# Optimization experiments

Hardware: AMD Instinct MI355X
Metric: run time of the kernel (lower is better)

## Reference

```python
import jax, jax.numpy as jnp
import numpy as np
import math

B, S, L, H, NH, FF, V = 32, 512, 12, 768, 12, 3072, 30522
DH = H // NH


def setup_inputs() -> dict:
    key = jax.random.key(0)
    ks = jax.random.split(key, 16)
    w = lambda k, shape: (jax.random.normal(k, shape, jnp.float32) * 0.02)
    return {
        "input_ids": jax.random.randint(ks[0], (B, S), 0, V, dtype=jnp.int32),
        "attention_mask": jax.random.uniform(ks[1], (B, S), jnp.float32),
        "word_emb": w(ks[2], (V, H)),
        "pos_emb": w(ks[3], (S, H)),
        "type_emb": w(ks[4], (H,)),
        "ln_emb_s": jnp.ones((H,), jnp.float32),
        "ln_emb_b": jnp.zeros((H,), jnp.float32),
        "Wq": w(ks[5], (L, H, H)), "bq": jnp.zeros((L, H), jnp.float32),
        "Wk": w(ks[6], (L, H, H)), "bk": jnp.zeros((L, H), jnp.float32),
        "Wv": w(ks[7], (L, H, H)), "bv": jnp.zeros((L, H), jnp.float32),
        "Wo": w(ks[8], (L, H, H)), "bo": jnp.zeros((L, H), jnp.float32),
        "ln1_s": jnp.ones((L, H), jnp.float32), "ln1_b": jnp.zeros((L, H), jnp.float32),
        "Wi": w(ks[9], (L, H, FF)), "bi": jnp.zeros((L, FF), jnp.float32),
        "Wf": w(ks[10], (L, FF, H)), "bf": jnp.zeros((L, H), jnp.float32),
        "ln2_s": jnp.ones((L, H), jnp.float32), "ln2_b": jnp.zeros((L, H), jnp.float32),
    }


def _ln(x, s, b):
    # BERT LayerNorm, eps=1e-12
    m = jnp.mean(x, -1, keepdims=True)
    v = jnp.mean((x - m) ** 2, -1, keepdims=True)
    return (x - m) * jax.lax.rsqrt(v + 1e-12) * s + b


def reference(input_ids, attention_mask, word_emb, pos_emb, type_emb,
              ln_emb_s, ln_emb_b, Wq, bq, Wk, bk, Wv, bv, Wo, bo,
              ln1_s, ln1_b, Wi, bi, Wf, bf, ln2_s, ln2_b):
    b, s = input_ids.shape
    scale = 1.0 / math.sqrt(DH)
    # Embeddings: word + position + (single) token-type, then LayerNorm
    h = word_emb[input_ids] + pos_emb[None, :s] + type_emb
    h = _ln(h, ln_emb_s, ln_emb_b)
    key_mask = attention_mask[:, None, None, :]  # [B,1,1,S], float

    def layer(h, p):
        wq, bq_, wk, bk_, wv, bv_, wo, bo_, l1s, l1b, wi, bi_, wf, bf_, l2s, l2b = p
        q = (jnp.einsum('bsd,de->bse', h, wq) + bq_).reshape(b, s, NH, DH)
        k = (jnp.einsum('bsd,de->bse', h, wk) + bk_).reshape(b, s, NH, DH)
        v = (jnp.einsum('bsd,de->bse', h, wv) + bv_).reshape(b, s, NH, DH)
        scores = jnp.einsum('bqhd,bkhd->bhqk', q, k) * scale
        probs = jax.nn.softmax(scores, axis=-1)
        # post-softmax masking + renormalization (the non-standard part)
        probs = probs * key_mask
        probs = probs / jnp.clip(jnp.sum(probs, -1, keepdims=True), 1e-9, None)
        ctx = jnp.einsum('bhqk,bkhd->bqhd', probs, v).reshape(b, s, H)
        attn_out = _ln(jnp.einsum('bsd,de->bse', ctx, wo) + bo_ + h, l1s, l1b)
        inter = jax.nn.gelu(jnp.einsum('bsd,df->bsf', attn_out, wi) + bi_, approximate=False)
        out = _ln(jnp.einsum('bsf,fd->bsd', inter, wf) + bf_ + attn_out, l2s, l2b)
        return out, None

    h, _ = jax.lax.scan(layer, h, (Wq, bq, Wk, bk, Wv, bv, Wo, bo,
                                   ln1_s, ln1_b, Wi, bi, Wf, bf, ln2_s, ln2_b))
    # masked mean pooling + L2 normalize (normalize=True)
    m = attention_mask[..., None]
    sent = jnp.sum(h * m, axis=1) / jnp.clip(jnp.sum(m, axis=1), 1e-6, None)
    sent = sent / jnp.clip(jnp.linalg.norm(sent, axis=-1, keepdims=True), 1e-12, None)
    return sent
```

## Files before the change

kernel.cpp:

```cpp
#include <hip/hip_runtime.h>
#include <hip/hip_bf16.h>
#include <math.h>

typedef __bf16 bf16;
typedef __bf16 bf16x8 __attribute__((ext_vector_type(8)));
typedef float  f32x4  __attribute__((ext_vector_type(4)));

#define B_  32
#define S_  512
#define H_  768
#define NH_ 12
#define DH_ 64
#define FF_ 3072
#define L_  12
#define M_  (B_*S_)
#define QKV_ 2304

#define KST 68
#define VST 516
#define PST 68

__device__ __forceinline__ void gload16(const bf16* g, bf16* l) {
  __builtin_amdgcn_global_load_lds(
      (const __attribute__((address_space(1))) void*)g,
      (__attribute__((address_space(3))) void*)l, 16, 0, 0);
}

__device__ __forceinline__ float fast_gelu(float x) {
  float z = x * 0.70710678118f;
  float s = fabsf(z);
  float t = __builtin_amdgcn_rcpf(1.0f + 0.3275911f * s);
  float p = t*(0.254829592f + t*(-0.284496736f + t*(1.421413741f +
            t*(-1.453152027f + t*1.061405429f))));
  float e = p * __expf(-s*s);
  float erfv = copysignf(1.0f - e, z);
  return 0.5f * x * (1.0f + erfv);
}

__global__ __launch_bounds__(512, 4) void gemm128(
    const bf16* __restrict__ A, const bf16* __restrict__ Bt,
    const float* __restrict__ bias, void* __restrict__ outp,
    int N, int K, int tiles_n, int epi)
{
  __shared__ bf16 As[128*64];
  __shared__ bf16 Bs[128*64];
  const int tid  = threadIdx.x;
  const int lane = tid & 63, wid = tid >> 6;
  const int wr = wid >> 2, wc = wid & 3;
  const int lrow = lane & 15, kgrp = lane >> 4;

  const int nwg = gridDim.x, orig = blockIdx.x;
  const int qc = nwg >> 3, rc = nwg & 7;
  const int xcd = orig & 7, lin = orig >> 3;
  const int wg = (xcd < rc ? xcd*(qc+1) : rc*(qc+1) + (xcd-rc)*qc) + lin;
  const int tm = wg / tiles_n, tn = wg % tiles_n;
  const size_t m0 = (size_t)tm * 128, n0 = (size_t)tn * 128;
  const int KT = K >> 6;

  const bf16* Ab = A  + m0 * K;
  const bf16* Bb = Bt + n0 * K;

  auto stage = [&](const bf16* gbase, bf16* ldsbase, int kt) {
#pragma unroll
    for (int j = 0; j < 2; ++j) {
      int lin2  = j*512 + tid;
      int prow  = lin2 >> 3;
      int pslot = lin2 & 7;
      int lslot = pslot ^ (prow & 7);
      const bf16* src = gbase + (size_t)prow * K + (size_t)kt*64 + lslot*8;
      bf16* dst = ldsbase + (size_t)(j*512 + (wid<<6))*8;
      gload16(src, dst);
    }
  };

  f32x4 acc[4][2] = {};

  for (int t = 0; t < KT; ++t) {
    __syncthreads();
    stage(Ab, As, t);
    stage(Bb, Bs, t);
    __syncthreads();
#pragma unroll
    for (int kk = 0; kk < 2; ++kk) {
      bf16x8 a[4], b[2];
#pragma unroll
      for (int m = 0; m < 4; ++m) {
        int row  = wr*64 + m*16 + lrow;
        int slot = (kk*4 + kgrp) ^ (lrow & 7);
        a[m] = *(const bf16x8*)&As[row*64 + slot*8];
      }
#pragma unroll
      for (int n = 0; n < 2; ++n) {
        int row  = wc*32 + n*16 + lrow;
        int slot = (kk*4 + kgrp) ^ (lrow & 7);
        b[n] = *(const bf16x8*)&Bs[row*64 + slot*8];
      }
#pragma unroll
      for (int m = 0; m < 4; ++m)
#pragma unroll
        for (int n = 0; n < 2; ++n)
          acc[m][n] = __builtin_amdgcn_mfma_f32_16x16x32_bf16(a[m], b[n], acc[m][n], 0, 0, 0);
    }
  }

#pragma unroll
  for (int m = 0; m < 4; ++m)
#pragma unroll
    for (int n = 0; n < 2; ++n) {
      int col = (int)n0 + wc*32 + n*16 + lrow;
      float bv = bias[col];
#pragma unroll
      for (int r = 0; r < 4; ++r) {
        int row = (int)m0 + wr*64 + m*16 + kgrp*4 + r;
        float x = acc[m][n][r] + bv;
        size_t idx = (size_t)row * N + col;
        if (epi == 1)      ((float*)outp)[idx] = x;
        else if (epi == 0) ((bf16*)outp)[idx]  = (bf16)x;
        else               ((bf16*)outp)[idx]  = (bf16)fast_gelu(x);
      }
    }
}

__global__ __launch_bounds__(256) void weight_prep(
    const float* __restrict__ Wq, const float* __restrict__ Wk,
    const float* __restrict__ Wv, const float* __restrict__ Wo,
    const float* __restrict__ Wi, const float* __restrict__ Wf,
    const float* __restrict__ bq, const float* __restrict__ bk,
    const float* __restrict__ bv,
    bf16* __restrict__ wqkv, bf16* __restrict__ wot,
    bf16* __restrict__ wit,  bf16* __restrict__ wft,
    float* __restrict__ qkbias)
{
  int bid = blockIdx.x;
  if (bid >= 1728) {
    int i = (bid - 1728)*256 + threadIdx.x;
    if (i < QKV_)
      qkbias[i] = (i < 768) ? bq[i] : (i < 1536 ? bk[i-768] : bv[i-1536]);
    return;
  }
  const float* W; bf16* Wt; int K, N, t;
  if (bid < 576) {
    K = 768; N = 768;
    if      (bid < 144) { W = Wq; Wt = wqkv;             t = bid; }
    else if (bid < 288) { W = Wk; Wt = wqkv + 768*768;   t = bid - 144; }
    else if (bid < 432) { W = Wv; Wt = wqkv + 2*768*768; t = bid - 288; }
    else                { W = Wo; Wt = wot;              t = bid - 432; }
  } else if (bid < 1152) { W = Wi; Wt = wit; K = 768;  N = 3072; t = bid - 576; }
  else                   { W = Wf; Wt = wft; K = 3072; N = 768;  t = bid - 1152; }
  const int kt = K >> 6;
  const int k0 = (t % kt)*64, n0 = (t / kt)*64;

  __shared__ bf16 T[64][65];
  int tx = threadIdx.x & 63, ty = threadIdx.x >> 6;
#pragma unroll
  for (int j = 0; j < 16; ++j) {
    int kk = j*4 + ty;
    T[kk][tx] = (bf16)W[(size_t)(k0+kk)*N + n0 + tx];
  }
  __syncthreads();
#pragma unroll
  for (int j = 0; j < 16; ++j) {
    int nn = j*4 + ty;
    Wt[(size_t)(n0+nn)*K + k0 + tx] = T[tx][nn];
  }
}

__device__ __forceinline__ void block_sum2(float& a, float& b, float* red) {
  int lane = threadIdx.x & 63, wid = threadIdx.x >> 6;
  for (int o = 32; o > 0; o >>= 1) { a += __shfl_xor(a, o); b += __shfl_xor(b, o); }
  if (lane == 0) { red[wid*2] = a; red[wid*2+1] = b; }
  __syncthreads();
  a = red[0] + red[2] + red[4] + red[6];
  b = red[1] + red[3] + red[5] + red[7];
  __syncthreads();
}

__global__ __launch_bounds__(256) void embed_ln(
    const int* __restrict__ ids, const float* __restrict__ we,
    const float* __restrict__ pe, const float* __restrict__ te,
    const float* __restrict__ gs, const float* __restrict__ gb,
    float* __restrict__ h32, bf16* __restrict__ hb)
{
  __shared__ float red[8];
  int row = blockIdx.x;
  int s = row & (S_-1);
  int id = ids[row];
  int t = threadIdx.x;
  float x[3], sum = 0.f, sq = 0.f;
#pragma unroll
  for (int j = 0; j < 3; ++j) {
    int c = t + j*256;
    float v = we[(size_t)id*H_ + c] + pe[(size_t)s*H_ + c] + te[c];
    x[j] = v; sum += v; sq += v*v;
  }
  block_sum2(sum, sq, red);
  float mean = sum * (1.f/H_);
  float var  = sq  * (1.f/H_) - mean*mean;
  float rstd = rsqrtf(fmaxf(var, 0.f) + 1e-12f);
#pragma unroll
  for (int j = 0; j < 3; ++j) {
    int c = t + j*256;
    float y = (x[j]-mean)*rstd*gs[c] + gb[c];
    h32[(size_t)row*H_ + c] = y;
    hb [(size_t)row*H_ + c] = (bf16)y;
  }
}

__global__ __launch_bounds__(256) void ln_res(
    const float* __restrict__ t32, const float* __restrict__ res,
    const float* __restrict__ gs, const float* __restrict__ gb,
    float* __restrict__ o32, bf16* __restrict__ ob)
{
  __shared__ float red[8];
  int row = blockIdx.x, t = threadIdx.x;
  float x[3], sum = 0.f, sq = 0.f;
#pragma unroll
  for (int j = 0; j < 3; ++j) {
    int c = t + j*256;
    float v = t32[(size_t)row*H_ + c] + res[(size_t)row*H_ + c];
    x[j] = v; sum += v; sq += v*v;
  }
  block_sum2(sum, sq, red);
  float mean = sum * (1.f/H_);
  float var  = sq  * (1.f/H_) - mean*mean;
  float rstd = rsqrtf(fmaxf(var, 0.f) + 1e-12f);
#pragma unroll
  for (int j = 0; j < 3; ++j) {
    int c = t + j*256;
    float y = (x[j]-mean)*rstd*gs[c] + gb[c];
    o32[(size_t)row*H_ + c] = y;
    ob [(size_t)row*H_ + c] = (bf16)y;
  }
}

__global__ __launch_bounds__(512, 2) void attn_kernel(
    const bf16* __restrict__ qkv, const float* __restrict__ mask,
    bf16* __restrict__ ctx)
{
  __shared__ bf16 Kl[S_*KST];
  __shared__ bf16 Vt[DH_*VST];
  __shared__ float mk[S_];
  __shared__ bf16 Pl[8][16*PST];
  int bid = blockIdx.x;
  int h = bid % NH_, b = bid / NH_;
  int tid = threadIdx.x, lane = tid & 63, wid = tid >> 6;
  int lrow = lane & 15, kgrp = lane >> 4;
  const bf16* Qb = qkv + (size_t)(b*S_)*QKV_        + h*DH_;
  const bf16* Kb = qkv + (size_t)(b*S_)*QKV_ + H_   + h*DH_;
  const bf16* Vb = qkv + (size_t)(b*S_)*QKV_ + 2*H_ + h*DH_;

  for (int it = 0; it < 8; ++it) {
    int slot = it*512 + tid;
    int s = slot >> 3, c8 = (slot & 7)*8;
    bf16x8 kv = *(const bf16x8*)&Kb[(size_t)s*QKV_ + c8];
#pragma unroll
    for (int i = 0; i < 8; ++i) kv[i] = (bf16)((float)kv[i] * 0.125f);
    *(bf16x8*)&Kl[s*KST + c8] = kv;
    bf16x8 v = *(const bf16x8*)&Vb[(size_t)s*QKV_ + c8];
#pragma unroll
    for (int i = 0; i < 8; ++i) Vt[(c8+i)*VST + s] = v[i];
  }
  mk[tid] = mask[b*S_ + tid];
  __syncthreads();

  for (int pass = 0; pass < 4; ++pass) {
    int q0 = pass*128 + wid*16;
    bf16x8 qa[2];
#pragma unroll
    for (int kc = 0; kc < 2; ++kc)
      qa[kc] = *(const bf16x8*)&Qb[(size_t)(q0 + lrow)*QKV_ + kc*32 + kgrp*8];
    f32x4 O[4] = {};
    float mrun[4], lrun[4];
#pragma unroll
    for (int r = 0; r < 4; ++r) { mrun[r] = -1e30f; lrun[r] = 0.f; }

    for (int c0 = 0; c0 < S_; c0 += 64) {
      f32x4 Sf[4] = {};
      __builtin_amdgcn_s_setprio(1);
#pragma unroll
      for (int kc = 0; kc < 2; ++kc)
#pragma unroll
        for (int sn = 0; sn < 4; ++sn) {
          bf16x8 kbv = *(const bf16x8*)&Kl[(c0 + sn*16 + lrow)*KST + kc*32 + kgrp*8];
          Sf[sn] = __builtin_amdgcn_mfma_f32_16x16x32_bf16(qa[kc], kbv, Sf[sn], 0, 0, 0);
        }
      __builtin_amdgcn_s_setprio(0);
      float cmax[4];
#pragma unroll
      for (int r = 0; r < 4; ++r) cmax[r] = -1e30f;
#pragma unroll
      for (int sn = 0; sn < 4; ++sn)
#pragma unroll
        for (int r = 0; r < 4; ++r)
          cmax[r] = fmaxf(cmax[r], Sf[sn][r]);
      for (int o = 1; o < 16; o <<= 1)
#pragma unroll
        for (int r = 0; r < 4; ++r) cmax[r] = fmaxf(cmax[r], __shfl_xor(cmax[r], o));
      float newm[4], fr[4], lsum[4];
#pragma unroll
      for (int r = 0; r < 4; ++r) {
        newm[r] = fmaxf(mrun[r], cmax[r]);
        fr[r]   = __expf(mrun[r] - newm[r]);
        lsum[r] = 0.f;
      }
#pragma unroll
      for (int sn = 0; sn < 4; ++sn) {
        float mkv = mk[c0 + sn*16 + lrow];
#pragma unroll
        for (int r = 0; r < 4; ++r) {
          float e = __expf(Sf[sn][r] - newm[r]) * mkv;
          bf16 eb = (bf16)e;
          lsum[r] += (float)eb;
          Pl[wid][(kgrp*4 + r)*PST + sn*16 + lrow] = eb;
        }
      }
#pragma unroll
      for (int on = 0; on < 4; ++on)
#pragma unroll
        for (int r = 0; r < 4; ++r) O[on][r] *= fr[r];
      asm volatile("s_waitcnt lgkmcnt(0)" ::: "memory");
      __builtin_amdgcn_sched_barrier(0);
      __builtin_amdgcn_s_setprio(1);
#pragma unroll
      for (int kc = 0; kc < 2; ++kc) {
        bf16x8 pa = *(const bf16x8*)&Pl[wid][lrow*PST + kc*32 + kgrp*8];
#pragma unroll
        for (int on = 0; on < 4; ++on) {
          bf16x8 vv = *(const bf16x8*)&Vt[(on*16 + lrow)*VST + c0 + kc*32 + kgrp*8];
          O[on] = __builtin_amdgcn_mfma_f32_16x16x32_bf16(pa, vv, O[on], 0, 0, 0);
        }
      }
      __builtin_amdgcn_s_setprio(0);
      for (int o = 1; o < 16; o <<= 1)
#pragma unroll
        for (int r = 0; r < 4; ++r) lsum[r] += __shfl_xor(lsum[r], o);
#pragma unroll
      for (int r = 0; r < 4; ++r) { lrun[r] = lrun[r]*fr[r] + lsum[r]; mrun[r] = newm[r]; }
    }
#pragma unroll
    for (int on = 0; on < 4; ++on)
#pragma unroll
      for (int r = 0; r < 4; ++r) {
        float val = O[on][r] / fmaxf(lrun[r], 1e-9f);
        int q = q0 + kgrp*4 + r;
        ctx[(size_t)(b*S_ + q)*H_ + h*DH_ + on*16 + lrow] = (bf16)val;
      }
  }
}

__global__ __launch_bounds__(256) void pool_norm(
    const float* __restrict__ h32, const float* __restrict__ mask,
    float* __restrict__ out)
{
  __shared__ float red[8];
  int b = blockIdx.x, t = threadIdx.x;
  float a0 = 0.f, a1 = 0.f, a2 = 0.f;
  for (int s = 0; s < S_; ++s) {
    float m = mask[b*S_ + s];
    const float* hp = &h32[((size_t)b*S_ + s)*H_];
    a0 += hp[t]*m; a1 += hp[t+256]*m; a2 += hp[t+512]*m;
  }
  float msum = mask[b*S_ + t] + mask[b*S_ + 256 + t];
  float dummy = 0.f;
  block_sum2(msum, dummy, red);
  float inv = 1.f / fmaxf(msum, 1e-6f);
  float s0 = a0*inv, s1 = a1*inv, s2 = a2*inv;
  float nrm = s0*s0 + s1*s1 + s2*s2;
  dummy = 0.f;
  block_sum2(nrm, dummy, red);
  float rn = 1.f / fmaxf(sqrtf(nrm), 1e-12f);
  out[b*H_ + t]       = s0*rn;
  out[b*H_ + t + 256] = s1*rn;
  out[b*H_ + t + 512] = s2*rn;
}

extern "C" void kernel_launch(void* const* d_in, const int* in_sizes, int n_in,
                              void* d_out, int out_size, void* d_ws, size_t ws_size,
                              hipStream_t stream)
{
  const int*   ids  = (const int*)  d_in[0];
  const float* mask = (const float*)d_in[1];
  const float* we   = (const float*)d_in[2];
  const float* pe   = (const float*)d_in[3];
  const float* te   = (const float*)d_in[4];
  const float* les  = (const float*)d_in[5];
  const float* leb  = (const float*)d_in[6];
  const float* Wq   = (const float*)d_in[7];
  const float* bq   = (const float*)d_in[8];
  const float* Wk   = (const float*)d_in[9];
  const float* bk   = (const float*)d_in[10];
  const float* Wv   = (const float*)d_in[11];
  const float* bv   = (const float*)d_in[12];
  const float* Wo   = (const float*)d_in[13];
  const float* bo   = (const float*)d_in[14];
  const float* l1s  = (const float*)d_in[15];
  const float* l1b  = (const float*)d_in[16];
  const float* Wi   = (const float*)d_in[17];
  const float* bi   = (const float*)d_in[18];
  const float* Wf   = (const float*)d_in[19];
  const float* bfp  = (const float*)d_in[20];
  const float* l2s  = (const float*)d_in[21];
  const float* l2b  = (const float*)d_in[22];

  char* p = (char*)d_ws;
  auto alloc = [&](size_t bytes) { char* q = p; p += (bytes + 255) & ~(size_t)255; return q; };
  bf16*  wqkv = (bf16*) alloc((size_t)QKV_*H_*2);
  bf16*  wot  = (bf16*) alloc((size_t)H_*H_*2);
  bf16*  wit  = (bf16*) alloc((size_t)H_*FF_*2);
  bf16*  wft  = (bf16*) alloc((size_t)H_*FF_*2);
  float* qkbias=(float*)alloc((size_t)QKV_*4);
  bf16*  hb   = (bf16*) alloc((size_t)M_*H_*2);
  float* h32  = (float*)alloc((size_t)M_*H_*4);
  float* a32  = (float*)alloc((size_t)M_*H_*4);
  float* tmp  = (float*)alloc((size_t)M_*H_*4);
  bf16*  qkvb = (bf16*) alloc((size_t)M_*QKV_*2);
  bf16*  cxb  = (bf16*) alloc((size_t)M_*H_*2);
  bf16*  inb  = (bf16*) alloc((size_t)M_*FF_*2);

  embed_ln<<<M_, 256, 0, stream>>>(ids, we, pe, te, les, leb, h32, hb);

  for (int l = 0; l < L_; ++l) {
    size_t wsq = (size_t)l*H_*H_;
    weight_prep<<<1737, 256, 0, stream>>>(
        Wq + wsq, Wk + wsq, Wv + wsq, Wo + wsq,
        Wi + (size_t)l*H_*FF_, Wf + (size_t)l*FF_*H_,
        bq + l*H_, bk + l*H_, bv + l*H_,
        wqkv, wot, wit, wft, qkbias);

    gemm128<<<128*(QKV_/128), 512, 0, stream>>>(hb,  wqkv, qkbias,      qkvb, QKV_, H_,  QKV_/128, 0);
    attn_kernel<<<B_*NH_, 512, 0, stream>>>(qkvb, mask, cxb);
    gemm128<<<128*(H_/128),  512, 0, stream>>>(cxb, wot, bo  + l*H_,  tmp,  H_,  H_,  H_/128,  1);
    ln_res<<<M_, 256, 0, stream>>>(tmp, h32, l1s + l*H_, l1b + l*H_, a32, hb);
    gemm128<<<128*(FF_/128), 512, 0, stream>>>(hb,  wit, bi  + l*FF_, inb,  FF_, H_,  FF_/128, 2);
    gemm128<<<128*(H_/128),  512, 0, stream>>>(inb, wft, bfp + l*H_,  tmp,  H_,  FF_, H_/128,  1);
    ln_res<<<M_, 256, 0, stream>>>(tmp, a32, l2s + l*H_, l2b + l*H_, h32, hb);
  }

  pool_norm<<<B_, 256, 0, stream>>>(h32, mask, (float*)d_out);
}
```

Measured before the change: 5.710 ms.

## Fuse residual add into GEMM epilogue, rebalance attention grid, lazy softmax rescale

```diff
diff --git a/kernel.cpp b/kernel.cpp
--- a/kernel.cpp
+++ b/kernel.cpp
@@ -39,8 +39,8 @@
 
 __global__ __launch_bounds__(512, 4) void gemm128(
     const bf16* __restrict__ A, const bf16* __restrict__ Bt,
-    const float* __restrict__ bias, void* __restrict__ outp,
-    int N, int K, int tiles_n, int epi)
+    const float* __restrict__ bias, const float* __restrict__ resid,
+    void* __restrict__ outp, int N, int K, int tiles_n, int epi)
 {
   __shared__ bf16 As[128*64];
   __shared__ bf16 Bs[128*64];
@@ -116,6 +116,7 @@
         size_t idx = (size_t)row * N + col;
         if (epi == 1)      ((float*)outp)[idx] = x;
         else if (epi == 0) ((bf16*)outp)[idx]  = (bf16)x;
+        else if (epi == 3) ((float*)outp)[idx] = x + resid[idx];
         else               ((bf16*)outp)[idx]  = (bf16)fast_gelu(x);
       }
     }
@@ -206,8 +207,8 @@
   }
 }
 
-__global__ __launch_bounds__(256) void ln_res(
-    const float* __restrict__ t32, const float* __restrict__ res,
+__global__ __launch_bounds__(256) void ln_single(
+    const float* __restrict__ t32,
     const float* __restrict__ gs, const float* __restrict__ gb,
     float* __restrict__ o32, bf16* __restrict__ ob)
 {
@@ -217,7 +218,7 @@
 #pragma unroll
   for (int j = 0; j < 3; ++j) {
     int c = t + j*256;
-    float v = t32[(size_t)row*H_ + c] + res[(size_t)row*H_ + c];
+    float v = t32[(size_t)row*H_ + c];
     x[j] = v; sum += v; sq += v*v;
   }
   block_sum2(sum, sq, red);
@@ -241,29 +242,36 @@
   __shared__ bf16 Vt[DH_*VST];
   __shared__ float mk[S_];
   __shared__ bf16 Pl[8][16*PST];
-  int bid = blockIdx.x;
-  int h = bid % NH_, b = bid / NH_;
   int tid = threadIdx.x, lane = tid & 63, wid = tid >> 6;
   int lrow = lane & 15, kgrp = lane >> 4;
-  const bf16* Qb = qkv + (size_t)(b*S_)*QKV_        + h*DH_;
-  const bf16* Kb = qkv + (size_t)(b*S_)*QKV_ + H_   + h*DH_;
-  const bf16* Vb = qkv + (size_t)(b*S_)*QKV_ + 2*H_ + h*DH_;
-
-  for (int it = 0; it < 8; ++it) {
-    int slot = it*512 + tid;
-    int s = slot >> 3, c8 = (slot & 7)*8;
-    bf16x8 kv = *(const bf16x8*)&Kb[(size_t)s*QKV_ + c8];
-#pragma unroll
-    for (int i = 0; i < 8; ++i) kv[i] = (bf16)((float)kv[i] * 0.125f);
-    *(bf16x8*)&Kl[s*KST + c8] = kv;
-    bf16x8 v = *(const bf16x8*)&Vb[(size_t)s*QKV_ + c8];
-#pragma unroll
-    for (int i = 0; i < 8; ++i) Vt[(c8+i)*VST + s] = v[i];
-  }
-  mk[tid] = mask[b*S_ + tid];
-  __syncthreads();
-
-  for (int pass = 0; pass < 4; ++pass) {
+  int cur_head = -1;
+
+  for (int u = 0; u < 6; ++u) {
+    int unit = blockIdx.x*6 + u;
+    int hh = unit >> 2, pass = unit & 3;
+    int b = hh / NH_, h = hh % NH_;
+    const bf16* Qb = qkv + (size_t)(b*S_)*QKV_ + h*DH_;
+
+    if (hh != cur_head) {
+      __syncthreads();
+      const bf16* Kb = qkv + (size_t)(b*S_)*QKV_ + H_   + h*DH_;
+      const bf16* Vb = qkv + (size_t)(b*S_)*QKV_ + 2*H_ + h*DH_;
+      for (int it = 0; it < 8; ++it) {
+        int slot = it*512 + tid;
+        int s = slot >> 3, c8 = (slot & 7)*8;
+        bf16x8 kv = *(const bf16x8*)&Kb[(size_t)s*QKV_ + c8];
+#pragma unroll
+        for (int i = 0; i < 8; ++i) kv[i] = (bf16)((float)kv[i] * 0.125f);
+        *(bf16x8*)&Kl[s*KST + c8] = kv;
+        bf16x8 v = *(const bf16x8*)&Vb[(size_t)s*QKV_ + c8];
+#pragma unroll
+        for (int i = 0; i < 8; ++i) Vt[(c8+i)*VST + s] = v[i];
+      }
+      mk[tid] = mask[b*S_ + tid];
+      cur_head = hh;
+      __syncthreads();
+    }
+
     int q0 = pass*128 + wid*16;
     bf16x8 qa[2];
 #pragma unroll
@@ -296,12 +304,21 @@
       for (int o = 1; o < 16; o <<= 1)
 #pragma unroll
         for (int r = 0; r < 4; ++r) cmax[r] = fmaxf(cmax[r], __shfl_xor(cmax[r], o));
+
+      bool small = (cmax[0] <= mrun[0]+8.f) && (cmax[1] <= mrun[1]+8.f) &&
+                   (cmax[2] <= mrun[2]+8.f) && (cmax[3] <= mrun[3]+8.f);
+      bool skip = __all(small);
       float newm[4], fr[4], lsum[4];
-#pragma unroll
-      for (int r = 0; r < 4; ++r) {
-        newm[r] = fmaxf(mrun[r], cmax[r]);
-        fr[r]   = __expf(mrun[r] - newm[r]);
-        lsum[r] = 0.f;
+      if (skip) {
+#pragma unroll
+        for (int r = 0; r < 4; ++r) { newm[r] = mrun[r]; fr[r] = 1.f; lsum[r] = 0.f; }
+      } else {
+#pragma unroll
+        for (int r = 0; r < 4; ++r) {
+          newm[r] = fmaxf(mrun[r], cmax[r]);
+          fr[r]   = __expf(mrun[r] - newm[r]);
+          lsum[r] = 0.f;
+        }
       }
 #pragma unroll
       for (int sn = 0; sn < 4; ++sn) {
@@ -314,10 +331,12 @@
           Pl[wid][(kgrp*4 + r)*PST + sn*16 + lrow] = eb;
         }
       }
-#pragma unroll
-      for (int on = 0; on < 4; ++on)
-#pragma unroll
-        for (int r = 0; r < 4; ++r) O[on][r] *= fr[r];
+      if (!skip) {
+#pragma unroll
+        for (int on = 0; on < 4; ++on)
+#pragma unroll
+          for (int r = 0; r < 4; ++r) O[on][r] *= fr[r];
+      }
       asm volatile("s_waitcnt lgkmcnt(0)" ::: "memory");
       __builtin_amdgcn_sched_barrier(0);
       __builtin_amdgcn_s_setprio(1);
@@ -427,13 +446,13 @@
         bq + l*H_, bk + l*H_, bv + l*H_,
         wqkv, wot, wit, wft, qkbias);
 
-    gemm128<<<128*(QKV_/128), 512, 0, stream>>>(hb,  wqkv, qkbias,      qkvb, QKV_, H_,  QKV_/128, 0);
-    attn_kernel<<<B_*NH_, 512, 0, stream>>>(qkvb, mask, cxb);
-    gemm128<<<128*(H_/128),  512, 0, stream>>>(cxb, wot, bo  + l*H_,  tmp,  H_,  H_,  H_/128,  1);
-    ln_res<<<M_, 256, 0, stream>>>(tmp, h32, l1s + l*H_, l1b + l*H_, a32, hb);
-    gemm128<<<128*(FF_/128), 512, 0, stream>>>(hb,  wit, bi  + l*FF_, inb,  FF_, H_,  FF_/128, 2);
-    gemm128<<<128*(H_/128),  512, 0, stream>>>(inb, wft, bfp + l*H_,  tmp,  H_,  FF_, H_/128,  1);
-    ln_res<<<M_, 256, 0, stream>>>(tmp, a32, l2s + l*H_, l2b + l*H_, h32, hb);
+    gemm128<<<128*(QKV_/128), 512, 0, stream>>>(hb,  wqkv, qkbias,     nullptr, qkvb, QKV_, H_,  QKV_/128, 0);
+    attn_kernel<<<256, 512, 0, stream>>>(qkvb, mask, cxb);
+    gemm128<<<128*(H_/128),  512, 0, stream>>>(cxb, wot, bo  + l*H_,  h32,     tmp,  H_,  H_,  H_/128,  3);
+    ln_single<<<M_, 256, 0, stream>>>(tmp, l1s + l*H_, l1b + l*H_, a32, hb);
+    gemm128<<<128*(FF_/128), 512, 0, stream>>>(hb,  wit, bi  + l*FF_, nullptr, inb,  FF_, H_,  FF_/128, 2);
+    gemm128<<<128*(H_/128),  512, 0, stream>>>(inb, wft, bfp + l*H_,  a32,     tmp,  H_,  FF_, H_/128,  3);
+    ln_single<<<M_, 256, 0, stream>>>(tmp, l2s + l*H_, l2b + l*H_, h32, hb);
   }
 
   pool_norm<<<B_, 256, 0, stream>>>(h32, mask, (float*)d_out);
```

Result: slower. 5.938 ms (+4.0%).
